# Kernel tuning notes

Hardware: AMD Instinct MI355X
Metric: run time of the kernel (lower is better)

## Reference

```python
import jax, jax.numpy as jnp
jax.config.update("jax_enable_x64", True)
import numpy as np

B, IN_DIM, OUT_DIM = 65536, 256, 256
SCALE = 100.0


def setup_inputs() -> dict:
    key = jax.random.key(0)
    k1, k2, k3 = jax.random.split(key, 3)
    c_x = jax.random.randint(k1, (B, IN_DIM), 0, 200, dtype=jnp.int64)
    weight = jax.random.normal(k2, (OUT_DIM, IN_DIM), dtype=jnp.float32)
    true_bias = jax.random.normal(k3, (OUT_DIM,), dtype=jnp.float32)
    in_scale = jnp.ones((1,), dtype=jnp.float32) * jnp.float32(SCALE)
    return {"c_x": c_x, "weight": weight, "true_bias": true_bias, "in_scale": in_scale}


def scale_round(x, scale):
    # torch.round(x * scale).long()
    return jnp.round(x * scale).astype(jnp.int64)


def reference(c_x, weight, true_bias, in_scale):
    scale = jnp.float32(SCALE)
    s = in_scale[0]
    # quantize weight (done in __init__ in the original) and bias (done per-forward)
    w_q = scale_round(weight, scale)                 # [OUT, IN] int64
    b_q = scale_round(true_bias, s * scale)          # [OUT] int64
    # fhe.matrix_product(W, x.T).T == x @ W.T, then add_matrix_vector adds bias per row
    out = jnp.matmul(c_x, w_q.T) + b_q[None, :]      # [B, OUT] int64
    return out, s * scale
```

## Files before the change

kernel.cpp:

```cpp
#include <hip/hip_runtime.h>
#include <hip/hip_bf16.h>

typedef _Float16 half8 __attribute__((ext_vector_type(8)));
typedef _Float16 half4 __attribute__((ext_vector_type(4)));
typedef float floatx4 __attribute__((ext_vector_type(4)));

#define IN_DIM 256
#define OUT_DIM 256
#define M_TILE 64
#define ROWSTR 264

__global__ void quant_kernel(const float* __restrict__ w,
                             const float* __restrict__ bias,
                             const float* __restrict__ in_scale,
                             _Float16* __restrict__ wq,
                             float* __restrict__ bq,
                             float* __restrict__ out_scalar) {
    int i = blockIdx.x * blockDim.x + threadIdx.x;
    if (i < OUT_DIM * IN_DIM) {
        wq[i] = (_Float16)rintf(w[i] * 100.0f);
    }
    if (i < OUT_DIM) {
        float s2 = in_scale[0] * 100.0f;
        bq[i] = rintf(bias[i] * s2);
    }
    if (i == 0 && out_scalar != nullptr) {
        out_scalar[0] = in_scale[0] * 100.0f;
    }
}

__global__ __launch_bounds__(256, 4) void gemm_kernel(const int* __restrict__ cx,
                                                      const _Float16* __restrict__ wq,
                                                      const float* __restrict__ bq,
                                                      float* __restrict__ out) {
    __shared__ _Float16 aT[M_TILE * ROWSTR];

    const int t = threadIdx.x;
    const size_t m0 = (size_t)blockIdx.x * M_TILE;

    const int* cbase = cx + m0 * IN_DIM;
#pragma unroll
    for (int i = 0; i < 16; ++i) {
        int flat = i * 1024 + t * 4;
        int4 v = *(const int4*)(cbase + flat);
        int row = flat >> 8;
        int col = flat & 255;
        half4 h;
        h.x = (_Float16)v.x; h.y = (_Float16)v.y;
        h.z = (_Float16)v.z; h.w = (_Float16)v.w;
        *(half4*)&aT[row * ROWSTR + col] = h;
    }
    __syncthreads();

    const int wave = t >> 6;
    const int lane = t & 63;
    const int m16  = lane & 15;
    const int quad = lane >> 4;
    const int n0   = wave * 64;

    floatx4 acc[4][4] = {};

#pragma unroll
    for (int ks = 0; ks < 8; ++ks) {
        const int kb = ks * 32 + quad * 8;
        half8 afr[4], bfr[4];
#pragma unroll
        for (int i = 0; i < 4; ++i)
            afr[i] = *(const half8*)&aT[(i * 16 + m16) * ROWSTR + kb];
#pragma unroll
        for (int j = 0; j < 4; ++j)
            bfr[j] = *(const half8*)(wq + (size_t)(n0 + j * 16 + m16) * IN_DIM + kb);
#pragma unroll
        for (int i = 0; i < 4; ++i)
#pragma unroll
            for (int j = 0; j < 4; ++j)
                acc[i][j] = __builtin_amdgcn_mfma_f32_16x16x32_f16(afr[i], bfr[j], acc[i][j], 0, 0, 0);
    }

#pragma unroll
    for (int j = 0; j < 4; ++j) {
        int col = n0 + j * 16 + m16;
        float bv = bq[col];
#pragma unroll
        for (int i = 0; i < 4; ++i) {
#pragma unroll
            for (int r = 0; r < 4; ++r) {
                size_t row = m0 + i * 16 + quad * 4 + r;
                out[row * OUT_DIM + col] = acc[i][j][r] + bv;
            }
        }
    }
}

extern "C" void kernel_launch(void* const* d_in, const int* in_sizes, int n_in,
                              void* d_out, int out_size, void* d_ws, size_t ws_size,
                              hipStream_t stream) {
    const int*   cx       = (const int*)d_in[0];
    const float* w        = (const float*)d_in[1];
    const float* bias     = (const float*)d_in[2];
    const float* in_scale = (const float*)d_in[3];
    float* out = (float*)d_out;

    _Float16* wq = (_Float16*)d_ws;
    float*    bq = (float*)((char*)d_ws + OUT_DIM * IN_DIM * 2);

    const int rows = in_sizes[0] / IN_DIM;
    const size_t gemm_elems = (size_t)rows * OUT_DIM;
    float* out_scalar = ((size_t)out_size > gemm_elems) ? (out + gemm_elems) : nullptr;

    quant_kernel<<<(OUT_DIM * IN_DIM + 255) / 256, 256, 0, stream>>>(
        w, bias, in_scale, wq, bq, out_scalar);

    gemm_kernel<<<rows / M_TILE, 256, 0, stream>>>(cx, wq, bq, out);
}
```

Baseline: 126.1 us.

## Pre-pack weights in MFMA fragment order and swap operands for vectorized output stores

The quantize kernel now writes the weight matrix in MFMA fragment order, so each lane's half8 load in the GEMM is a fully coalesced contiguous read. The MFMA operands are swapped: weights become the A operand and the LDS-staged activations become B. Each lane then holds four consecutive output columns and can write them as float4 stores, replacing strided scalar stores. The quant kernel now runs with fewer threads, each doing 8 elements, and bias is loaded as a vector.

```diff
diff --git a/kernel.cpp b/kernel.cpp
--- a/kernel.cpp
+++ b/kernel.cpp
@@ -1,5 +1,4 @@
 #include <hip/hip_runtime.h>
-#include <hip/hip_bf16.h>
 
 typedef _Float16 half8 __attribute__((ext_vector_type(8)));
 typedef _Float16 half4 __attribute__((ext_vector_type(4)));
@@ -13,27 +12,36 @@
 __global__ void quant_kernel(const float* __restrict__ w,
                              const float* __restrict__ bias,
                              const float* __restrict__ in_scale,
-                             _Float16* __restrict__ wq,
+                             _Float16* __restrict__ wqp,
                              float* __restrict__ bq,
                              float* __restrict__ out_scalar) {
-    int i = blockIdx.x * blockDim.x + threadIdx.x;
-    if (i < OUT_DIM * IN_DIM) {
-        wq[i] = (_Float16)rintf(w[i] * 100.0f);
+    int t = blockIdx.x * blockDim.x + threadIdx.x;
+    if (t < (OUT_DIM * IN_DIM) / 8) {
+        int lane = t & 63;
+        int ks   = (t >> 6) & 7;
+        int ct   = t >> 9;
+        int row  = ct * 16 + (lane & 15);
+        int k0   = ks * 32 + (lane >> 4) * 8;
+        const float* src = w + row * IN_DIM + k0;
+        half8 h;
+#pragma unroll
+        for (int e = 0; e < 8; ++e)
+            h[e] = (_Float16)rintf(src[e] * 100.0f);
+        *((half8*)wqp + t) = h;
     }
-    if (i < OUT_DIM) {
+    if (t < OUT_DIM) {
         float s2 = in_scale[0] * 100.0f;
-        bq[i] = rintf(bias[i] * s2);
+        bq[t] = rintf(bias[t] * s2);
     }
-    if (i == 0 && out_scalar != nullptr) {
+    if (t == 0 && out_scalar != nullptr)
         out_scalar[0] = in_scale[0] * 100.0f;
-    }
 }
 
 __global__ __launch_bounds__(256, 4) void gemm_kernel(const int* __restrict__ cx,
-                                                      const _Float16* __restrict__ wq,
+                                                      const _Float16* __restrict__ wqp,
                                                       const float* __restrict__ bq,
                                                       float* __restrict__ out) {
-    __shared__ _Float16 aT[M_TILE * ROWSTR];
+    __shared__ _Float16 cT[M_TILE * ROWSTR];
 
     const int t = threadIdx.x;
     const size_t m0 = (size_t)blockIdx.x * M_TILE;
@@ -48,7 +56,7 @@
         half4 h;
         h.x = (_Float16)v.x; h.y = (_Float16)v.y;
         h.z = (_Float16)v.z; h.w = (_Float16)v.w;
-        *(half4*)&aT[row * ROWSTR + col] = h;
+        *(half4*)&cT[row * ROWSTR + col] = h;
     }
     __syncthreads();
 
@@ -56,20 +64,20 @@
     const int lane = t & 63;
     const int m16  = lane & 15;
     const int quad = lane >> 4;
-    const int n0   = wave * 64;
 
     floatx4 acc[4][4] = {};
 
+    const half8* wbase = (const half8*)wqp;
 #pragma unroll
     for (int ks = 0; ks < 8; ++ks) {
-        const int kb = ks * 32 + quad * 8;
         half8 afr[4], bfr[4];
 #pragma unroll
         for (int i = 0; i < 4; ++i)
-            afr[i] = *(const half8*)&aT[(i * 16 + m16) * ROWSTR + kb];
+            afr[i] = wbase[((wave * 4 + i) * 8 + ks) * 64 + lane];
+        const int kb = ks * 32 + quad * 8;
 #pragma unroll
         for (int j = 0; j < 4; ++j)
-            bfr[j] = *(const half8*)(wq + (size_t)(n0 + j * 16 + m16) * IN_DIM + kb);
+            bfr[j] = *(const half8*)&cT[(j * 16 + m16) * ROWSTR + kb];
 #pragma unroll
         for (int i = 0; i < 4; ++i)
 #pragma unroll
@@ -78,16 +86,14 @@
     }
 
 #pragma unroll
-    for (int j = 0; j < 4; ++j) {
-        int col = n0 + j * 16 + m16;
-        float bv = bq[col];
+    for (int i = 0; i < 4; ++i) {
+        int col = wave * 64 + i * 16 + quad * 4;
+        floatx4 bv = *(const floatx4*)(bq + col);
 #pragma unroll
-        for (int i = 0; i < 4; ++i) {
-#pragma unroll
-            for (int r = 0; r < 4; ++r) {
-                size_t row = m0 + i * 16 + quad * 4 + r;
-                out[row * OUT_DIM + col] = acc[i][j][r] + bv;
-            }
+        for (int j = 0; j < 4; ++j) {
+            size_t row = m0 + j * 16 + m16;
+            floatx4 v = acc[i][j] + bv;
+            *(floatx4*)(out + row * OUT_DIM + col) = v;
         }
     }
 }
@@ -101,15 +107,13 @@
     const float* in_scale = (const float*)d_in[3];
     float* out = (float*)d_out;
 
-    _Float16* wq = (_Float16*)d_ws;
-    float*    bq = (float*)((char*)d_ws + OUT_DIM * IN_DIM * 2);
+    _Float16* wqp = (_Float16*)d_ws;
+    float*    bq  = (float*)((char*)d_ws + OUT_DIM * IN_DIM * 2);
 
     const int rows = in_sizes[0] / IN_DIM;
     const size_t gemm_elems = (size_t)rows * OUT_DIM;
     float* out_scalar = ((size_t)out_size > gemm_elems) ? (out + gemm_elems) : nullptr;
 
-    quant_kernel<<<(OUT_DIM * IN_DIM + 255) / 256, 256, 0, stream>>>(
-        w, bias, in_scale, wq, bq, out_scalar);
-
-    gemm_kernel<<<rows / M_TILE, 256, 0, stream>>>(cx, wq, bq, out);
+    quant_kernel<<<32, 256, 0, stream>>>(w, bias, in_scale, wqp, bq, out_scalar);
+    gemm_kernel<<<rows / M_TILE, 256, 0, stream>>>(cx, wqp, bq, out);
 }
```

Result: no change. 123.9 us (-1.7%).
